# Performance work log

Hardware: AMD Instinct MI355X
Metric: run time of the kernel (lower is better)

The kernel has to match this reference:

```python
import jax, jax.numpy as jnp
import numpy as np

D_MODEL = 1024
N_HEAD = 16
D_K = 64
D_V = 64
B, S = 4, 2048


def setup_inputs() -> dict:
    key = jax.random.key(0)
    ks = jax.random.split(key, 7)
    scale = 1.0 / np.sqrt(D_MODEL)
    return {
        "q": jax.random.normal(ks[0], (B, S, D_MODEL), jnp.float32),
        "k": jax.random.normal(ks[1], (B, S, D_MODEL), jnp.float32),
        "v": jax.random.normal(ks[2], (B, S, D_MODEL), jnp.float32),
        "Wq": jax.random.normal(ks[3], (D_MODEL, N_HEAD * D_K), jnp.float32) * scale,
        "Wk": jax.random.normal(ks[4], (D_MODEL, N_HEAD * D_K), jnp.float32) * scale,
        "Wv": jax.random.normal(ks[5], (D_MODEL, N_HEAD * D_V), jnp.float32) * scale,
        "Wo": jax.random.normal(ks[6], (N_HEAD * D_V, D_MODEL), jnp.float32) * scale,
    }


def reference(q, k, v, Wq, Wk, Wv, Wo):
    B_, Sq, _ = q.shape
    Sk = k.shape[1]
    # projections (Linear, no bias) -> [B, S, H, d] -> [B, H, S, d]
    qh = (q @ Wq).reshape(B_, Sq, N_HEAD, D_K).transpose(0, 2, 1, 3)
    kh = (k @ Wk).reshape(B_, Sk, N_HEAD, D_K).transpose(0, 2, 1, 3)
    vh = (v @ Wv).reshape(B_, Sk, N_HEAD, D_V).transpose(0, 2, 1, 3)
    # scaled dot-product attention (no mask, dropout=0/eval)
    scores = jnp.einsum("bhqd,bhkd->bhqk", qh, kh) / jnp.sqrt(jnp.float32(D_K))
    attn = jax.nn.softmax(scores, axis=-1)
    ctx = jnp.einsum("bhqk,bhkd->bhqd", attn, vh)  # [B,H,Sq,D_V]
    ctx = ctx.transpose(0, 2, 1, 3).reshape(B_, Sq, N_HEAD * D_V)
    return ctx @ Wo
```

## Files before the change

### kernel.cpp

```cpp
#include <hip/hip_runtime.h>
#include <hip/hip_bf16.h>

typedef unsigned short u16;
typedef __attribute__((ext_vector_type(8))) short bf16x8;
typedef __attribute__((ext_vector_type(4))) float f32x4;
typedef __attribute__((ext_vector_type(16))) float f32x16;
typedef __attribute__((ext_vector_type(4))) u16 u16x4;
typedef __attribute__((ext_vector_type(2))) int i32x2;
typedef __attribute__((ext_vector_type(4))) int i32x4;

#define DEV __device__ __forceinline__

constexpr int B_ = 4, S_ = 2048, H_ = 16, DK_ = 64, DM_ = 1024;
constexpr int M_ = B_ * S_;

DEV u16 f2bf(float x) {
  union { float f; unsigned u; } v; v.f = x;
  return (u16)((v.u + 0x7fffu + ((v.u >> 16) & 1u)) >> 16);
}

DEV bf16x8 ld16(const u16* p) { return *(const bf16x8*)p; }

DEV void g2l16(const void* g, void* l) {
  __builtin_amdgcn_global_load_lds((const __attribute__((address_space(1))) void*)g,
                                   (__attribute__((address_space(3))) void*)l, 16, 0, 0);
}

DEV int cvtpk(float lo, float hi) {
  int r;
  asm("v_cvt_pk_bf16_f32 %0, %1, %2" : "=v"(r) : "v"(lo), "v"(hi));
  return r;
}

DEV i32x2 pl32swap(int a, int b) {
  return __builtin_amdgcn_permlane32_swap(a, b, false, false);
}

DEV float asf(int x) { return __builtin_bit_cast(float, x); }
DEV int asi(float x) { return __builtin_bit_cast(int, x); }

__global__ __launch_bounds__(256) void wtrans_kernel(const float* __restrict__ W,
                                                     u16* __restrict__ Wt) {
  __shared__ u16 t[64][68];
  const int r0 = blockIdx.y * 64, c0 = blockIdx.x * 64;
  const int lr = threadIdx.x >> 4;
  const int lc = (threadIdx.x & 15) * 4;
#pragma unroll
  for (int i = 0; i < 4; ++i) {
    int row = i * 16 + lr;
    float4 v = *(const float4*)(W + (size_t)(r0 + row) * DM_ + c0 + lc);
    t[lc + 0][row] = f2bf(v.x); t[lc + 1][row] = f2bf(v.y);
    t[lc + 2][row] = f2bf(v.z); t[lc + 3][row] = f2bf(v.w);
  }
  __syncthreads();
#pragma unroll
  for (int i = 0; i < 4; ++i) {
    int c = i * 16 + lr;
    u16x4 o; o[0] = t[c][lc]; o[1] = t[c][lc + 1]; o[2] = t[c][lc + 2]; o[3] = t[c][lc + 3];
    *(u16x4*)(Wt + (size_t)(c0 + c) * DM_ + r0 + lc) = o;
  }
}

template <int KIND>
__global__ __launch_bounds__(256, 2) void gemm128(const float* __restrict__ x0f,
                                                  const float* __restrict__ x1f,
                                                  const float* __restrict__ x2f,
                                                  const u16* __restrict__ xb,
                                                  const u16* __restrict__ w0,
                                                  const u16* __restrict__ w1,
                                                  const u16* __restrict__ w2,
                                                  void* __restrict__ o0,
                                                  void* __restrict__ o1,
                                                  void* __restrict__ o2) {
  constexpr int K = 1024, NK = 16;
  __shared__ u16 As[2][8192];
  __shared__ u16 Bs[2][8192];
  const int tid = threadIdx.x;
  const int w = tid >> 6, lane = tid & 63;
  const int l15 = lane & 15, lg = (lane >> 4) & 3;
  const int sr = tid >> 3;
  const int c8 = tid & 7;
  const int cg = c8 ^ (sr & 7);

  const int wg = blockIdx.x;
  const int cpx = gridDim.x >> 3;
  const int idx = (wg & 7) * cpx + (wg >> 3);
  const int sel = (KIND == 0) ? (idx >> 9) : 0;
  const int rid = (KIND == 0) ? (idx & 511) : idx;
  const int mblk = rid >> 3, nblk = rid & 7;
  const int m0 = mblk * 128, n0 = nblk * 128;

  const float* Xf = nullptr;
  const u16* Wt;
  if (KIND == 0) {
    Xf = sel == 0 ? x0f : sel == 1 ? x1f : x2f;
    Wt = sel == 0 ? w0 : sel == 1 ? w1 : w2;
  } else {
    Wt = w0;
  }

  const int wm = (w >> 1) * 64, wn = (w & 1) * 64;
  f32x4 acc[4][4] = {};

  {
#pragma unroll
    for (int j = 0; j < 4; ++j) {
      int r = j * 32 + sr;
      g2l16(Wt + (size_t)(n0 + r) * K + cg * 8, &Bs[0][(j * 32 + 8 * w) * 64]);
    }
    if (KIND == 0) {
#pragma unroll
      for (int j = 0; j < 4; ++j) {
        int r = j * 32 + sr;
        const float* src = Xf + (size_t)(m0 + r) * K + c8 * 8;
        float4 u = *(const float4*)src, v2 = *(const float4*)(src + 4);
        i32x4 pk = {cvtpk(u.x, u.y), cvtpk(u.z, u.w), cvtpk(v2.x, v2.y), cvtpk(v2.z, v2.w)};
        *(i32x4*)(&As[0][r * 64 + cg * 8]) = pk;
      }
    } else {
#pragma unroll
      for (int j = 0; j < 4; ++j) {
        int r = j * 32 + sr;
        g2l16(xb + (size_t)(m0 + r) * K + cg * 8, &As[0][(j * 32 + 8 * w) * 64]);
      }
    }
  }

  for (int g = 0; g < NK; ++g) {
    asm volatile("s_waitcnt vmcnt(0) lgkmcnt(0)" ::: "memory");
    __builtin_amdgcn_s_barrier();
    asm volatile("" ::: "memory");
    const int rs = g & 1, ws2 = (g + 1) & 1;
    const bool st = (g + 1) < NK;
    const int kt1 = (g + 1) * 64;

    float4 au[4], av[4];
    if (st) {
      if (KIND == 0) {
#pragma unroll
        for (int j = 0; j < 4; ++j) {
          int r = j * 32 + sr;
          const float* src = Xf + (size_t)(m0 + r) * K + kt1 + c8 * 8;
          au[j] = *(const float4*)src;
          av[j] = *(const float4*)(src + 4);
        }
      }
#pragma unroll
      for (int j = 0; j < 4; ++j) {
        int r = j * 32 + sr;
        g2l16(Wt + (size_t)(n0 + r) * K + kt1 + cg * 8, &Bs[ws2][(j * 32 + 8 * w) * 64]);
      }
      if (KIND == 1) {
#pragma unroll
        for (int j = 0; j < 4; ++j) {
          int r = j * 32 + sr;
          g2l16(xb + (size_t)(m0 + r) * K + kt1 + cg * 8, &As[ws2][(j * 32 + 8 * w) * 64]);
        }
      }
    }

#pragma unroll
    for (int kk = 0; kk < 2; ++kk) {
      bf16x8 af[4], bfr[4];
      const int ck = (kk * 4 + lg) ^ (l15 & 7);
#pragma unroll
      for (int mf = 0; mf < 4; ++mf)
        af[mf] = ld16(&As[rs][(wm + mf * 16 + l15) * 64 + ck * 8]);
#pragma unroll
      for (int nf = 0; nf < 4; ++nf)
        bfr[nf] = ld16(&Bs[rs][(wn + nf * 16 + l15) * 64 + ck * 8]);
      __builtin_amdgcn_s_setprio(1);
#pragma unroll
      for (int mf = 0; mf < 4; ++mf)
#pragma unroll
        for (int nf = 0; nf < 4; ++nf)
          acc[mf][nf] = __builtin_amdgcn_mfma_f32_16x16x32_bf16(af[mf], bfr[nf], acc[mf][nf], 0, 0, 0);
      __builtin_amdgcn_s_setprio(0);
    }

    if (KIND == 0 && st) {
      __builtin_amdgcn_sched_barrier(0);
#pragma unroll
      for (int j = 0; j < 4; ++j) {
        int r = j * 32 + sr;
        float4 u = au[j], v2 = av[j];
        i32x4 pk = {cvtpk(u.x, u.y), cvtpk(u.z, u.w), cvtpk(v2.x, v2.y), cvtpk(v2.z, v2.w)};
        *(i32x4*)(&As[ws2][r * 64 + cg * 8]) = pk;
      }
    }
  }

#pragma unroll
  for (int mf = 0; mf < 4; ++mf)
#pragma unroll
    for (int nf = 0; nf < 4; ++nf) {
      if (KIND == 0 && sel == 2) {
        int m = m0 + wm + mf * 16 + lg * 4;
        int n = n0 + wn + nf * 16 + l15;
        int b = m >> 11, s = m & 2047;
        int h = n >> 6, d = n & 63;
        u16x4 o;
#pragma unroll
        for (int r = 0; r < 4; ++r) o[r] = f2bf(acc[mf][nf][r]);
        *(u16x4*)((u16*)o2 + ((size_t)(b * H_ + h) * DK_ + d) * S_ + s) = o;
      } else if (KIND == 0) {
        u16* op = (u16*)(sel == 0 ? o0 : o1);
#pragma unroll
        for (int r = 0; r < 4; ++r) {
          int m = m0 + wm + mf * 16 + lg * 4 + r;
          int n = n0 + wn + nf * 16 + l15;
          int b = m >> 11, s = m & 2047;
          int h = n >> 6, d = n & 63;
          op[((size_t)(b * H_ + h) * S_ + s) * DK_ + d] = f2bf(acc[mf][nf][r]);
        }
      } else {
#pragma unroll
        for (int r = 0; r < 4; ++r) {
          int m = m0 + wm + mf * 16 + lg * 4 + r;
          int n = n0 + wn + nf * 16 + l15;
          ((float*)o0)[(size_t)m * DM_ + n] = acc[mf][nf][r];
        }
      }
    }
}

__global__ __launch_bounds__(256, 4) void attn_kernel(const u16* __restrict__ Qh,
                                                      const u16* __restrict__ Kh,
                                                      const u16* __restrict__ Vt,
                                                      u16* __restrict__ ctx) {
  __shared__ u16 KV[2][2][4096];
  const int tid = threadIdx.x;
  const int lane = tid & 63, w = tid >> 6;
  const int l31 = lane & 31, hi = lane >> 5;
  const int bh = blockIdx.y;
  const int q0 = blockIdx.x * 128 + w * 32;

  const u16* Qb = Qh + (size_t)bh * S_ * DK_;
  const u16* Kb = Kh + (size_t)bh * S_ * DK_;
  const u16* Vb = Vt + (size_t)bh * DK_ * S_;

  const int srow = tid >> 3;
  const int cs = (tid & 7) ^ (srow & 7);
  const int dstoff = w * 512;

  bf16x8 qf[4];
#pragma unroll
  for (int ds = 0; ds < 4; ++ds)
    qf[ds] = ld16(Qb + (size_t)(q0 + l31) * DK_ + ds * 16 + hi * 8);

  f32x16 accO[2] = {};
  float mreg = -1e30f, lsum = 0.f;
  const float SC = 0.125f * 1.44269504088896f;
  const int swz = (l31 & 7);

#pragma unroll
  for (int j = 0; j < 2; ++j) {
    int r = j * 32 + srow;
    g2l16(Kb + (size_t)r * DK_ + cs * 8, &KV[0][0][j * 2048 + dstoff]);
    g2l16(Vb + (size_t)r * S_ + cs * 8, &KV[0][1][j * 2048 + dstoff]);
  }

  for (int i = 0; i < 32; ++i) {
    const int cur = i & 1, nxt = cur ^ 1;
    __syncthreads();
    if (i < 31) {
      const int kvn = (i + 1) * 64;
#pragma unroll
      for (int j = 0; j < 2; ++j) {
        int r = j * 32 + srow;
        g2l16(Kb + (size_t)(kvn + r) * DK_ + cs * 8, &KV[nxt][0][j * 2048 + dstoff]);
        g2l16(Vb + (size_t)r * S_ + kvn + cs * 8, &KV[nxt][1][j * 2048 + dstoff]);
      }
    }

    f32x16 accS[2] = {};
    __builtin_amdgcn_s_setprio(1);
#pragma unroll
    for (int t = 0; t < 2; ++t)
#pragma unroll
      for (int ds = 0; ds < 4; ++ds) {
        bf16x8 kf = ld16(&KV[cur][0][(t * 32 + l31) * 64 + (((ds * 2 + hi) ^ swz) * 8)]);
        accS[t] = __builtin_amdgcn_mfma_f32_32x32x16_bf16(kf, qf[ds], accS[t], 0, 0, 0);
      }
    __builtin_amdgcn_s_setprio(0);

    float a[8];
#pragma unroll
    for (int r = 0; r < 8; ++r)
      a[r] = fmaxf(fmaxf(accS[0][r], accS[1][r]), fmaxf(accS[0][r + 8], accS[1][r + 8]));
#pragma unroll
    for (int s = 4; s; s >>= 1)
#pragma unroll
      for (int r = 0; r < s; ++r) a[r] = fmaxf(a[r], a[r + s]);
    i32x2 mm = pl32swap(asi(a[0]), asi(a[0]));
    float mx = fmaxf(asf(mm.x), asf(mm.y)) * SC;
    if (__any(mx > mreg + 8.f)) {
      float mnew = fmaxf(mreg, mx);
      float scl = exp2f(mreg - mnew);
      mreg = mnew;
      lsum *= scl;
#pragma unroll
      for (int r = 0; r < 16; ++r) { accO[0][r] *= scl; accO[1][r] *= scl; }
    }
#pragma unroll
    for (int t = 0; t < 2; ++t)
#pragma unroll
      for (int r = 0; r < 16; ++r)
        accS[t][r] = exp2f(fmaf(accS[t][r], SC, -mreg));
#pragma unroll
    for (int r = 0; r < 8; ++r)
      a[r] = (accS[0][r] + accS[1][r]) + (accS[0][r + 8] + accS[1][r + 8]);
#pragma unroll
    for (int s = 4; s; s >>= 1)
#pragma unroll
      for (int r = 0; r < s; ++r) a[r] += a[r + s];
    i32x2 ss = pl32swap(asi(a[0]), asi(a[0]));
    lsum += asf(ss.x) + asf(ss.y);

    bf16x8 pb[4];
#pragma unroll
    for (int t = 0; t < 2; ++t) {
      i32x2 sA = pl32swap(cvtpk(accS[t][0], accS[t][1]), cvtpk(accS[t][4], accS[t][5]));
      i32x2 sB = pl32swap(cvtpk(accS[t][2], accS[t][3]), cvtpk(accS[t][6], accS[t][7]));
      i32x2 sC = pl32swap(cvtpk(accS[t][8], accS[t][9]), cvtpk(accS[t][12], accS[t][13]));
      i32x2 sD = pl32swap(cvtpk(accS[t][10], accS[t][11]), cvtpk(accS[t][14], accS[t][15]));
      union { i32x4 i; bf16x8 h; } u0, u1;
      u0.i = (i32x4){sA.x, sB.x, sA.y, sB.y};
      u1.i = (i32x4){sC.x, sD.x, sC.y, sD.y};
      pb[2 * t] = u0.h;
      pb[2 * t + 1] = u1.h;
    }

    __builtin_amdgcn_s_setprio(1);
#pragma unroll
    for (int ks = 0; ks < 4; ++ks)
#pragma unroll
      for (int dh = 0; dh < 2; ++dh) {
        bf16x8 vf = ld16(&KV[cur][1][(dh * 32 + l31) * 64 + (((ks * 2 + hi) ^ swz) * 8)]);
        accO[dh] = __builtin_amdgcn_mfma_f32_32x32x16_bf16(vf, pb[ks], accO[dh], 0, 0, 0);
      }
    __builtin_amdgcn_s_setprio(0);
  }

  const float inv = 1.f / lsum;
  const int b = bh >> 4, h = bh & 15;
  u16* crow = ctx + ((size_t)b * S_ + q0 + l31) * DM_ + h * DK_;
#pragma unroll
  for (int dh = 0; dh < 2; ++dh)
#pragma unroll
    for (int g = 0; g < 4; ++g) {
      u16x4 o;
#pragma unroll
      for (int r = 0; r < 4; ++r) o[r] = f2bf(accO[dh][g * 4 + r] * inv);
      *(u16x4*)(crow + dh * 32 + g * 8 + hi * 4) = o;
    }
}

extern "C" void kernel_launch(void* const* d_in, const int* in_sizes, int n_in,
                              void* d_out, int out_size, void* d_ws, size_t ws_size,
                              hipStream_t stream) {
  const float* q  = (const float*)d_in[0];
  const float* k  = (const float*)d_in[1];
  const float* v  = (const float*)d_in[2];
  const float* Wq = (const float*)d_in[3];
  const float* Wk = (const float*)d_in[4];
  const float* Wv = (const float*)d_in[5];
  const float* Wo = (const float*)d_in[6];

  char* ws = (char*)d_ws;
  const size_t SZX = (size_t)M_ * DM_ * 2;
  const size_t SZW = (size_t)DM_ * DM_ * 2;
  u16* Wqt = (u16*)(ws);
  u16* Wkt = (u16*)(ws + SZW);
  u16* Wvt = (u16*)(ws + 2 * SZW);
  u16* Wot = (u16*)(ws + 3 * SZW);
  u16* Qh  = (u16*)(ws + 4 * SZW);
  u16* Kh  = (u16*)(ws + 4 * SZW + SZX);
  u16* Vt  = (u16*)(ws + 4 * SZW + 2 * SZX);
  u16* ctx = (u16*)(ws + 4 * SZW + 3 * SZX);

  wtrans_kernel<<<dim3(16, 16), 256, 0, stream>>>(Wq, Wqt);
  wtrans_kernel<<<dim3(16, 16), 256, 0, stream>>>(Wk, Wkt);
  wtrans_kernel<<<dim3(16, 16), 256, 0, stream>>>(Wv, Wvt);
  wtrans_kernel<<<dim3(16, 16), 256, 0, stream>>>(Wo, Wot);

  gemm128<0><<<dim3(1536), 256, 0, stream>>>(q, k, v, nullptr, Wqt, Wkt, Wvt, Qh, Kh, Vt);

  attn_kernel<<<dim3(16, 64), 256, 0, stream>>>(Qh, Kh, Vt, ctx);

  gemm128<1><<<dim3(512), 256, 0, stream>>>(nullptr, nullptr, nullptr, ctx,
                                            Wot, nullptr, nullptr, d_out, nullptr, nullptr);
}
```

Baseline: 388.8 us.

## Pre-convert activations to bf16 and run projection GEMMs separately with async LDS loads

Drops the fused fp32-load-and-convert path from the QKV projection GEMM. Each activation (q, k, v) is first converted to bf16 by a standalone elementwise kernel into a shared workspace buffer, then a per-projection GEMM streams both operands straight into LDS with global_load_lds. This removes the register staging and conversion work from the GEMM main loop, at the cost of extra global traffic (an fp32 read plus a bf16 write and re-read per input), three separate projection launches instead of one wide launch, and serialization through the reused buffer.

```diff
diff --git a/kernel.cpp b/kernel.cpp
--- a/kernel.cpp
+++ b/kernel.cpp
@@ -39,6 +39,14 @@
 DEV float asf(int x) { return __builtin_bit_cast(float, x); }
 DEV int asi(float x) { return __builtin_bit_cast(int, x); }
 
+__global__ __launch_bounds__(256) void cvt_kernel(const float* __restrict__ in,
+                                                  u16* __restrict__ out) {
+  int i = (blockIdx.x * 256 + threadIdx.x) * 4;
+  float4 v = *(const float4*)(in + i);
+  u16x4 o; o[0] = f2bf(v.x); o[1] = f2bf(v.y); o[2] = f2bf(v.z); o[3] = f2bf(v.w);
+  *(u16x4*)(out + i) = o;
+}
+
 __global__ __launch_bounds__(256) void wtrans_kernel(const float* __restrict__ W,
                                                      u16* __restrict__ Wt) {
   __shared__ u16 t[64][68];
@@ -61,17 +69,10 @@
   }
 }
 
-template <int KIND>
-__global__ __launch_bounds__(256, 2) void gemm128(const float* __restrict__ x0f,
-                                                  const float* __restrict__ x1f,
-                                                  const float* __restrict__ x2f,
-                                                  const u16* __restrict__ xb,
-                                                  const u16* __restrict__ w0,
-                                                  const u16* __restrict__ w1,
-                                                  const u16* __restrict__ w2,
-                                                  void* __restrict__ o0,
-                                                  void* __restrict__ o1,
-                                                  void* __restrict__ o2) {
+template <int OUT_MODE>
+__global__ __launch_bounds__(256, 2) void gemm128b(const u16* __restrict__ X,
+                                                   const u16* __restrict__ Wt,
+                                                   void* __restrict__ outp) {
   constexpr int K = 1024, NK = 16;
   __shared__ u16 As[2][8192];
   __shared__ u16 Bs[2][8192];
@@ -85,45 +86,17 @@
   const int wg = blockIdx.x;
   const int cpx = gridDim.x >> 3;
   const int idx = (wg & 7) * cpx + (wg >> 3);
-  const int sel = (KIND == 0) ? (idx >> 9) : 0;
-  const int rid = (KIND == 0) ? (idx & 511) : idx;
-  const int mblk = rid >> 3, nblk = rid & 7;
+  const int mblk = idx >> 3, nblk = idx & 7;
   const int m0 = mblk * 128, n0 = nblk * 128;
-
-  const float* Xf = nullptr;
-  const u16* Wt;
-  if (KIND == 0) {
-    Xf = sel == 0 ? x0f : sel == 1 ? x1f : x2f;
-    Wt = sel == 0 ? w0 : sel == 1 ? w1 : w2;
-  } else {
-    Wt = w0;
-  }
 
   const int wm = (w >> 1) * 64, wn = (w & 1) * 64;
   f32x4 acc[4][4] = {};
 
-  {
-#pragma unroll
-    for (int j = 0; j < 4; ++j) {
-      int r = j * 32 + sr;
-      g2l16(Wt + (size_t)(n0 + r) * K + cg * 8, &Bs[0][(j * 32 + 8 * w) * 64]);
-    }
-    if (KIND == 0) {
-#pragma unroll
-      for (int j = 0; j < 4; ++j) {
-        int r = j * 32 + sr;
-        const float* src = Xf + (size_t)(m0 + r) * K + c8 * 8;
-        float4 u = *(const float4*)src, v2 = *(const float4*)(src + 4);
-        i32x4 pk = {cvtpk(u.x, u.y), cvtpk(u.z, u.w), cvtpk(v2.x, v2.y), cvtpk(v2.z, v2.w)};
-        *(i32x4*)(&As[0][r * 64 + cg * 8]) = pk;
-      }
-    } else {
-#pragma unroll
-      for (int j = 0; j < 4; ++j) {
-        int r = j * 32 + sr;
-        g2l16(xb + (size_t)(m0 + r) * K + cg * 8, &As[0][(j * 32 + 8 * w) * 64]);
-      }
-    }
+#pragma unroll
+  for (int j = 0; j < 4; ++j) {
+    int r = j * 32 + sr;
+    g2l16(Wt + (size_t)(n0 + r) * K + cg * 8, &Bs[0][(j * 32 + 8 * w) * 64]);
+    g2l16(X + (size_t)(m0 + r) * K + cg * 8, &As[0][(j * 32 + 8 * w) * 64]);
   }
 
   for (int g = 0; g < NK; ++g) {
@@ -134,28 +107,12 @@
     const bool st = (g + 1) < NK;
     const int kt1 = (g + 1) * 64;
 
-    float4 au[4], av[4];
     if (st) {
-      if (KIND == 0) {
-#pragma unroll
-        for (int j = 0; j < 4; ++j) {
-          int r = j * 32 + sr;
-          const float* src = Xf + (size_t)(m0 + r) * K + kt1 + c8 * 8;
-          au[j] = *(const float4*)src;
-          av[j] = *(const float4*)(src + 4);
-        }
-      }
 #pragma unroll
       for (int j = 0; j < 4; ++j) {
         int r = j * 32 + sr;
         g2l16(Wt + (size_t)(n0 + r) * K + kt1 + cg * 8, &Bs[ws2][(j * 32 + 8 * w) * 64]);
-      }
-      if (KIND == 1) {
-#pragma unroll
-        for (int j = 0; j < 4; ++j) {
-          int r = j * 32 + sr;
-          g2l16(xb + (size_t)(m0 + r) * K + kt1 + cg * 8, &As[ws2][(j * 32 + 8 * w) * 64]);
-        }
+        g2l16(X + (size_t)(m0 + r) * K + kt1 + cg * 8, &As[ws2][(j * 32 + 8 * w) * 64]);
       }
     }
 
@@ -177,24 +134,13 @@
           acc[mf][nf] = __builtin_amdgcn_mfma_f32_16x16x32_bf16(af[mf], bfr[nf], acc[mf][nf], 0, 0, 0);
       __builtin_amdgcn_s_setprio(0);
     }
-
-    if (KIND == 0 && st) {
-      __builtin_amdgcn_sched_barrier(0);
-#pragma unroll
-      for (int j = 0; j < 4; ++j) {
-        int r = j * 32 + sr;
-        float4 u = au[j], v2 = av[j];
-        i32x4 pk = {cvtpk(u.x, u.y), cvtpk(u.z, u.w), cvtpk(v2.x, v2.y), cvtpk(v2.z, v2.w)};
-        *(i32x4*)(&As[ws2][r * 64 + cg * 8]) = pk;
-      }
-    }
   }
 
 #pragma unroll
   for (int mf = 0; mf < 4; ++mf)
 #pragma unroll
     for (int nf = 0; nf < 4; ++nf) {
-      if (KIND == 0 && sel == 2) {
+      if (OUT_MODE == 2) {
         int m = m0 + wm + mf * 16 + lg * 4;
         int n = n0 + wn + nf * 16 + l15;
         int b = m >> 11, s = m & 2047;
@@ -202,23 +148,22 @@
         u16x4 o;
 #pragma unroll
         for (int r = 0; r < 4; ++r) o[r] = f2bf(acc[mf][nf][r]);
-        *(u16x4*)((u16*)o2 + ((size_t)(b * H_ + h) * DK_ + d) * S_ + s) = o;
-      } else if (KIND == 0) {
-        u16* op = (u16*)(sel == 0 ? o0 : o1);
+        *(u16x4*)((u16*)outp + ((size_t)(b * H_ + h) * DK_ + d) * S_ + s) = o;
+      } else if (OUT_MODE == 1) {
 #pragma unroll
         for (int r = 0; r < 4; ++r) {
           int m = m0 + wm + mf * 16 + lg * 4 + r;
           int n = n0 + wn + nf * 16 + l15;
           int b = m >> 11, s = m & 2047;
           int h = n >> 6, d = n & 63;
-          op[((size_t)(b * H_ + h) * S_ + s) * DK_ + d] = f2bf(acc[mf][nf][r]);
+          ((u16*)outp)[((size_t)(b * H_ + h) * S_ + s) * DK_ + d] = f2bf(acc[mf][nf][r]);
         }
       } else {
 #pragma unroll
         for (int r = 0; r < 4; ++r) {
           int m = m0 + wm + mf * 16 + lg * 4 + r;
           int n = n0 + wn + nf * 16 + l15;
-          ((float*)o0)[(size_t)m * DM_ + n] = acc[mf][nf][r];
+          ((float*)outp)[(size_t)m * DM_ + n] = acc[mf][nf][r];
         }
       }
     }
@@ -374,20 +319,25 @@
   u16* Wkt = (u16*)(ws + SZW);
   u16* Wvt = (u16*)(ws + 2 * SZW);
   u16* Wot = (u16*)(ws + 3 * SZW);
-  u16* Qh  = (u16*)(ws + 4 * SZW);
-  u16* Kh  = (u16*)(ws + 4 * SZW + SZX);
-  u16* Vt  = (u16*)(ws + 4 * SZW + 2 * SZX);
-  u16* ctx = (u16*)(ws + 4 * SZW + 3 * SZX);
+  u16* xb  = (u16*)(ws + 4 * SZW);
+  u16* Qh  = (u16*)(ws + 4 * SZW + SZX);
+  u16* Kh  = (u16*)(ws + 4 * SZW + 2 * SZX);
+  u16* Vt  = (u16*)(ws + 4 * SZW + 3 * SZX);
+  u16* ctx = xb;
 
   wtrans_kernel<<<dim3(16, 16), 256, 0, stream>>>(Wq, Wqt);
   wtrans_kernel<<<dim3(16, 16), 256, 0, stream>>>(Wk, Wkt);
   wtrans_kernel<<<dim3(16, 16), 256, 0, stream>>>(Wv, Wvt);
   wtrans_kernel<<<dim3(16, 16), 256, 0, stream>>>(Wo, Wot);
 
-  gemm128<0><<<dim3(1536), 256, 0, stream>>>(q, k, v, nullptr, Wqt, Wkt, Wvt, Qh, Kh, Vt);
+  cvt_kernel<<<8192, 256, 0, stream>>>(q, xb);
+  gemm128b<1><<<dim3(512), 256, 0, stream>>>(xb, Wqt, Qh);
+  cvt_kernel<<<8192, 256, 0, stream>>>(k, xb);
+  gemm128b<1><<<dim3(512), 256, 0, stream>>>(xb, Wkt, Kh);
+  cvt_kernel<<<8192, 256, 0, stream>>>(v, xb);
+  gemm128b<2><<<dim3(512), 256, 0, stream>>>(xb, Wvt, Vt);
 
   attn_kernel<<<dim3(16, 64), 256, 0, stream>>>(Qh, Kh, Vt, ctx);
 
-  gemm128<1><<<dim3(512), 256, 0, stream>>>(nullptr, nullptr, nullptr, ctx,
-                                            Wot, nullptr, nullptr, d_out, nullptr, nullptr);
-}
+  gemm128b<0><<<dim3(512), 256, 0, stream>>>(ctx, Wot, d_out);
+}
```

After: 364.2 us. -6.3%, faster.
